# Performance work log

Hardware: AMD Instinct MI355X
Metric: run time of the kernel (lower is better)

The kernel has to match this reference:

```python
import jax, jax.numpy as jnp
import numpy as np

B, C_IN, C_KEY, C_VAL, C_OUT = 1, 64, 32, 64, 64
H = W = D = 64
SCALE = 8


def setup_inputs() -> dict:
    key = jax.random.key(0)
    ks = jax.random.split(key, 4)
    init = lambda k, shape, fan: jax.random.normal(k, shape, jnp.float32) * (fan ** -0.5)
    return {
        "x": jax.random.normal(ks[0], (B, C_IN, H, W, D), jnp.float32),
        "w_key": init(ks[1], (C_KEY, C_IN), C_IN),
        "b_key": jnp.zeros((C_KEY,), jnp.float32),
        "w_value": init(ks[2], (C_VAL, C_IN), C_IN),
        "b_value": jnp.zeros((C_VAL,), jnp.float32),
        "w_out": init(ks[3], (C_OUT, C_VAL), C_VAL),
        "b_out": jnp.zeros((C_OUT,), jnp.float32),
        "scale": SCALE,
    }


def _proj(t, wgt, bias):
    # 1x1x1 Conv3d == pointwise channel matmul
    return jnp.einsum('bchwd,oc->bohwd', t, wgt) + bias[None, :, None, None, None]


def _windows(t, s):
    # [B,C,H,W,D] -> [B, s^3 windows, hb*wb*db tokens, C]
    b, c, h, w, d = t.shape
    hb, wb, db = h // s, w // s, d // s
    t = t.reshape(b, c, s, hb, s, wb, s, db)
    t = t.transpose(0, 2, 4, 6, 3, 5, 7, 1)
    return t.reshape(b, s * s * s, hb * wb * db, c), (hb, wb, db)


def _unwindows(t, s, blk):
    hb, wb, db = blk
    b, c = t.shape[0], t.shape[-1]
    t = t.reshape(b, s, s, s, hb, wb, db, c)
    t = t.transpose(0, 7, 1, 4, 2, 5, 3, 6)
    return t.reshape(b, c, s * hb, s * wb, s * db)


def reference(x, w_key, b_key, w_value, b_value, w_out, b_out, scale):
    # f_query = f_key (shared module in the original)
    k_full = _proj(x, w_key, b_key)
    v_full = _proj(x, w_value, b_value)
    qw, blk = _windows(k_full, scale)
    kw = qw  # shared projection -> query == key
    vw, _ = _windows(v_full, scale)
    sim = jnp.einsum('bnlc,bnmc->bnlm', qw, kw) * (qw.shape[-1] ** -0.5)
    sim = jax.nn.softmax(sim, axis=-1)
    ctx = jnp.einsum('bnlm,bnmc->bnlc', sim, vw)
    ctx = _unwindows(ctx, scale, blk)
    return _proj(ctx, w_out, b_out)
```

## Files before the change

### kernel.cpp

```cpp
#include <hip/hip_runtime.h>

typedef unsigned short u16;
typedef __bf16 bf16x8 __attribute__((ext_vector_type(8)));
typedef float f32x16 __attribute__((ext_vector_type(16)));

union B8 { bf16x8 v; u16 s[8]; unsigned u[4]; uint4 u4; };

__device__ __forceinline__ unsigned cvtpk(float a, float b) {
    unsigned r;
    asm("v_cvt_pk_bf16_f32 %0, %1, %2" : "=v"(r) : "v"(a), "v"(b));
    return r;
}
__device__ __forceinline__ float ex2(float x) { return __builtin_amdgcn_exp2f(x); }
__device__ __forceinline__ void swap32(unsigned &a, unsigned &b) {
    asm("v_permlane32_swap_b32 %0, %1" : "+v"(a), "+v"(b));
}
__device__ __forceinline__ B8 load_w8(const float* __restrict__ p, float s) {
    float4 lo = ((const float4*)p)[0];
    float4 hi = ((const float4*)p)[1];
    B8 r;
    r.u[0] = cvtpk(lo.x * s, lo.y * s);
    r.u[1] = cvtpk(lo.z * s, lo.w * s);
    r.u[2] = cvtpk(hi.x * s, hi.y * s);
    r.u[3] = cvtpk(hi.z * s, hi.w * s);
    return r;
}
__device__ __forceinline__ f32x16 mfma32(const B8 a, const B8 b, f32x16 c) {
    return __builtin_amdgcn_mfma_f32_32x32x16_bf16(a.v, b.v, c, 0, 0, 0);
}
__device__ __forceinline__ int kidx(int row, int sl) {
    return row * 32 + (((sl ^ (row >> 1)) & 3) << 3);
}
__device__ __forceinline__ void build_b(const float* p, B8& b0, B8& b1) {
    unsigned c0 = cvtpk(p[0], p[1]),   c1 = cvtpk(p[2], p[3]);
    unsigned c2 = cvtpk(p[4], p[5]),   c3 = cvtpk(p[6], p[7]);
    unsigned c4 = cvtpk(p[8], p[9]),   c5 = cvtpk(p[10], p[11]);
    unsigned c6 = cvtpk(p[12], p[13]), c7 = cvtpk(p[14], p[15]);
    swap32(c0, c2); swap32(c1, c3); swap32(c4, c6); swap32(c5, c7);
    b0.u[0] = c0; b0.u[1] = c1; b0.u[2] = c2; b0.u[3] = c3;
    b1.u[0] = c4; b1.u[1] = c5; b1.u[2] = c6; b1.u[3] = c7;
}

#define VOFF 16384
#define XOFF 49664
#define NSM  68096

__global__ __launch_bounds__(512, 1)
void psab_fused(const float* __restrict__ x,
                const float* __restrict__ wk, const float* __restrict__ bk,
                const float* __restrict__ wv, const float* __restrict__ bv,
                const float* __restrict__ wo, const float* __restrict__ bo,
                float* __restrict__ out)
{
    __shared__ __align__(16) u16 smem[NSM];
    const int t    = threadIdx.x;
    const int lane = t & 63;
    const int wid  = t >> 6;
    const int cl   = lane & 31;
    const int h5   = lane >> 5;

    const int bid = blockIdx.x;
    const int n   = (bid & 7) * 64 + (bid >> 3);
    const int sh = n >> 6, sw = (n >> 3) & 7, sd = n & 7;
    const size_t base_vox = (size_t)(sh * 8) * 4096 + (size_t)(sw * 8) * 64 + (size_t)(sd * 8);

    const float WSC = 0.50506330f;

    B8 wkB[4], wvB[2][4];
#pragma unroll
    for (int kc = 0; kc < 4; ++kc)
        wkB[kc] = load_w8(wk + cl * 64 + kc * 16 + h5 * 8, WSC);
#pragma unroll
    for (int nb = 0; nb < 2; ++nb)
#pragma unroll
        for (int kc = 0; kc < 4; ++kc)
            wvB[nb][kc] = load_w8(wv + (nb * 32 + cl) * 64 + kc * 16 + h5 * 8, 1.0f);
    const float kbias = bk[cl] * WSC;
    const float vbias[2] = { bv[cl], bv[32 + cl] };

    const f32x16 z16 = {0,0,0,0,0,0,0,0,0,0,0,0,0,0,0,0};

    const int cS = t & 63;
    const int r2 = t >> 6;
    float4 L4[4], H4[4];
#define LDX(cc)                                                                              \
    _Pragma("unroll")                                                                        \
    for (int i = 0; i < 4; ++i) {                                                            \
        const float* gp = x + (size_t)cS * 262144 + base_vox + ((cc) * 4 + i) * 4096 + r2 * 64; \
        L4[i] = ((const float4*)gp)[0];                                                      \
        H4[i] = ((const float4*)gp)[1];                                                      \
    }
#define STX()                                                                                \
    _Pragma("unroll")                                                                        \
    for (int i = 0; i < 4; ++i) {                                                            \
        unsigned a0 = cvtpk(L4[i].x, L4[i].y), a1 = cvtpk(L4[i].z, L4[i].w);                 \
        unsigned a2 = cvtpk(H4[i].x, H4[i].y), a3 = cvtpk(H4[i].z, H4[i].w);                 \
        u16* xp = &smem[XOFF + (i * 64 + r2 * 8) * 72 + cS];                                 \
        xp[0 * 72] = (u16)a0; xp[1 * 72] = (u16)(a0 >> 16);                                  \
        xp[2 * 72] = (u16)a1; xp[3 * 72] = (u16)(a1 >> 16);                                  \
        xp[4 * 72] = (u16)a2; xp[5 * 72] = (u16)(a2 >> 16);                                  \
        xp[6 * 72] = (u16)a3; xp[7 * 72] = (u16)(a3 >> 16);                                  \
    }

    LDX(0)
    STX()
    __syncthreads();
    LDX(1)

#pragma unroll
    for (int cc = 0; cc < 2; ++cc) {
        const int tokb = cc * 256 + wid * 32;
        B8 ax[4];
#pragma unroll
        for (int kc = 0; kc < 4; ++kc)
            ax[kc].u4 = *(const uint4*)&smem[XOFF + (wid * 32 + cl) * 72 + kc * 16 + h5 * 8];
        f32x16 kd = mfma32(ax[0], wkB[0], z16);
        kd = mfma32(ax[1], wkB[1], kd);
        kd = mfma32(ax[2], wkB[2], kd);
        kd = mfma32(ax[3], wkB[3], kd);
#pragma unroll
        for (int r = 0; r < 16; ++r) {
            const int row = tokb + (r & 3) + 8 * (r >> 2) + 4 * h5;
            smem[kidx(row, cl >> 3) + (cl & 7)] = (u16)cvtpk(kd[r] + kbias, kd[r] + kbias);
        }
#pragma unroll
        for (int nb = 0; nb < 2; ++nb) {
            f32x16 vd = mfma32(ax[0], wvB[nb][0], z16);
            vd = mfma32(ax[1], wvB[nb][1], vd);
            vd = mfma32(ax[2], wvB[nb][2], vd);
            vd = mfma32(ax[3], wvB[nb][3], vd);
            const int cv = nb * 32 + cl;
            const float vb = vbias[nb];
#pragma unroll
            for (int rq = 0; rq < 4; ++rq) {
                uint2 pk;
                pk.x = cvtpk(vd[rq * 4 + 0] + vb, vd[rq * 4 + 1] + vb);
                pk.y = cvtpk(vd[rq * 4 + 2] + vb, vd[rq * 4 + 3] + vb);
                *(uint2*)&smem[VOFF + cv * 520 + tokb + rq * 8 + 4 * h5] = pk;
            }
        }
        if (cc == 0) {
            __syncthreads();
            STX()
            __syncthreads();
        }
    }
    __syncthreads();

    B8 qB[2][2];
#pragma unroll
    for (int qb = 0; qb < 2; ++qb)
#pragma unroll
        for (int kc = 0; kc < 2; ++kc)
            qB[qb][kc].u4 = *(const uint4*)&smem[kidx(wid * 64 + qb * 32 + cl, 2 * kc + h5)];

    f32x16 ctx00 = z16, ctx01 = z16, ctx10 = z16, ctx11 = z16;
    float lsum0 = 0.f, lsum1 = 0.f;

#pragma unroll 2
    for (int ci = 0; ci < 16; ++ci) {
        const int m0 = ci * 32;
        B8 kA0, kA1, va00, va01, va10, va11;
        kA0.u4 = *(const uint4*)&smem[kidx(m0 + cl, h5)];
        kA1.u4 = *(const uint4*)&smem[kidx(m0 + cl, 2 + h5)];
        va00.u4 = *(const uint4*)&smem[VOFF + cl * 520 + m0 + h5 * 8];
        va01.u4 = *(const uint4*)&smem[VOFF + cl * 520 + m0 + 16 + h5 * 8];
        va10.u4 = *(const uint4*)&smem[VOFF + (32 + cl) * 520 + m0 + h5 * 8];
        va11.u4 = *(const uint4*)&smem[VOFF + (32 + cl) * 520 + m0 + 16 + h5 * 8];

        f32x16 s0 = mfma32(kA0, qB[0][0], z16);
        s0 = mfma32(kA1, qB[0][1], s0);
        f32x16 s1 = mfma32(kA0, qB[1][0], z16);
        s1 = mfma32(kA1, qB[1][1], s1);

        float p[16];
        B8 pb00, pb01, pb10, pb11;
#pragma unroll
        for (int i = 0; i < 16; ++i) p[i] = ex2(s0[i]);
        lsum0 += (((p[0]+p[1])+(p[2]+p[3]))+((p[4]+p[5])+(p[6]+p[7])))
               + (((p[8]+p[9])+(p[10]+p[11]))+((p[12]+p[13])+(p[14]+p[15])));
        build_b(p, pb00, pb01);
#pragma unroll
        for (int i = 0; i < 16; ++i) p[i] = ex2(s1[i]);
        lsum1 += (((p[0]+p[1])+(p[2]+p[3]))+((p[4]+p[5])+(p[6]+p[7])))
               + (((p[8]+p[9])+(p[10]+p[11]))+((p[12]+p[13])+(p[14]+p[15])));
        build_b(p, pb10, pb11);

        ctx00 = mfma32(va00, pb00, ctx00); ctx00 = mfma32(va01, pb01, ctx00);
        ctx10 = mfma32(va10, pb00, ctx10); ctx10 = mfma32(va11, pb01, ctx10);
        ctx01 = mfma32(va00, pb10, ctx01); ctx01 = mfma32(va01, pb11, ctx01);
        ctx11 = mfma32(va10, pb10, ctx11); ctx11 = mfma32(va11, pb11, ctx11);
    }

    lsum0 += __shfl_xor(lsum0, 32);
    lsum1 += __shfl_xor(lsum1, 32);
    const float inv0 = 1.0f / lsum0;
    const float inv1 = 1.0f / lsum1;

    B8 aw[2][4];
#pragma unroll
    for (int cob = 0; cob < 2; ++cob)
#pragma unroll
        for (int kc = 0; kc < 4; ++kc)
            aw[cob][kc] = load_w8(wo + (cob * 32 + cl) * 64 + kc * 16 + h5 * 8, 1.0f);

    float pn[16];
    B8 cq0[4], cq1[4];
#pragma unroll
    for (int i = 0; i < 16; ++i) pn[i] = ctx00[i] * inv0;
    build_b(pn, cq0[0], cq0[1]);
#pragma unroll
    for (int i = 0; i < 16; ++i) pn[i] = ctx10[i] * inv0;
    build_b(pn, cq0[2], cq0[3]);
#pragma unroll
    for (int i = 0; i < 16; ++i) pn[i] = ctx01[i] * inv1;
    build_b(pn, cq1[0], cq1[1]);
#pragma unroll
    for (int i = 0; i < 16; ++i) pn[i] = ctx11[i] * inv1;
    build_b(pn, cq1[2], cq1[3]);

    __syncthreads();

    float* fout = (float*)((char*)smem + wid * 16384);
#pragma unroll
    for (int cob = 0; cob < 2; ++cob) {
        f32x16 od0 = mfma32(aw[cob][0], cq0[0], z16);
        od0 = mfma32(aw[cob][1], cq0[1], od0);
        od0 = mfma32(aw[cob][2], cq0[2], od0);
        od0 = mfma32(aw[cob][3], cq0[3], od0);
        f32x16 od1 = mfma32(aw[cob][0], cq1[0], z16);
        od1 = mfma32(aw[cob][1], cq1[1], od1);
        od1 = mfma32(aw[cob][2], cq1[2], od1);
        od1 = mfma32(aw[cob][3], cq1[3], od1);
#pragma unroll
        for (int rq = 0; rq < 4; ++rq) {
            const float4 b4 = *(const float4*)(bo + cob * 32 + rq * 8 + h5 * 4);
            const float bb[4] = { b4.x, b4.y, b4.z, b4.w };
#pragma unroll
            for (int i = 0; i < 4; ++i) {
                const int row = cob * 32 + rq * 8 + h5 * 4 + i;
                fout[row * 64 + cl]      = od0[rq * 4 + i] + bb[i];
                fout[row * 64 + 32 + cl] = od1[rq * 4 + i] + bb[i];
            }
        }
    }

    float* outw = out + base_vox + (size_t)wid * 4096;
    const int lq = lane >> 4, lr = lane & 15;
#pragma unroll
    for (int it = 0; it < 16; ++it) {
        const int co = it * 4 + lq;
        const float4 v4 = *(const float4*)&fout[co * 64 + lr * 4];
        const int wb = lr >> 1, db0 = (lr & 1) * 4;
        *(float4*)&outw[(size_t)co * 262144 + wb * 64 + db0] = v4;
    }
}

extern "C" void kernel_launch(void* const* d_in, const int* in_sizes, int n_in,
                              void* d_out, int out_size, void* d_ws, size_t ws_size,
                              hipStream_t stream) {
    const float* x  = (const float*)d_in[0];
    const float* wk = (const float*)d_in[1];
    const float* bk = (const float*)d_in[2];
    const float* wv = (const float*)d_in[3];
    const float* bv = (const float*)d_in[4];
    const float* wo = (const float*)d_in[5];
    const float* bo = (const float*)d_in[6];
    float* o = (float*)d_out;
    psab_fused<<<dim3(512), dim3(512), 0, stream>>>(x, wk, bk, wv, bv, wo, bo, o);
}
```

Before: 72.34 us.

## Double block to 1024 threads, split K/V projection across wave pairs

Launches 1024 threads per block, so each wave handles 32 query rows instead of 64. In the projection phase, wave pairs divide the work: even waves compute K and odd waves compute V. The change also adds s_setprio around the MFMA groups and moves the output bias add into the store loop. It aims to raise wave-level parallelism and latency hiding, at the cost of more barrier participants and duplicated X fragment loads.

```diff
diff --git a/kernel.cpp b/kernel.cpp
--- a/kernel.cpp
+++ b/kernel.cpp
@@ -45,7 +45,7 @@
 #define XOFF 49664
 #define NSM  68096
 
-__global__ __launch_bounds__(512, 1)
+__global__ __launch_bounds__(1024, 4)
 void psab_fused(const float* __restrict__ x,
                 const float* __restrict__ wk, const float* __restrict__ bk,
                 const float* __restrict__ wv, const float* __restrict__ bv,
@@ -66,40 +66,53 @@
 
     const float WSC = 0.50506330f;
 
-    B8 wkB[4], wvB[2][4];
-#pragma unroll
-    for (int kc = 0; kc < 4; ++kc)
-        wkB[kc] = load_w8(wk + cl * 64 + kc * 16 + h5 * 8, WSC);
-#pragma unroll
-    for (int nb = 0; nb < 2; ++nb)
+    const int pair = wid >> 1;
+    const int kv   = wid & 1;
+
+    B8 wB[8];
+    float bkv[16];
+    float vb0 = 0.f, vb1 = 0.f;
+    if (kv == 0) {
 #pragma unroll
         for (int kc = 0; kc < 4; ++kc)
-            wvB[nb][kc] = load_w8(wv + (nb * 32 + cl) * 64 + kc * 16 + h5 * 8, 1.0f);
-    const float kbias = bk[cl] * WSC;
-    const float vbias[2] = { bv[cl], bv[32 + cl] };
+            wB[kc] = load_w8(wk + cl * 64 + kc * 16 + h5 * 8, WSC);
+#pragma unroll
+        for (int r = 0; r < 16; ++r)
+            bkv[r] = bk[(r & 3) + 8 * (r >> 2) + 4 * h5] * WSC;
+    } else {
+#pragma unroll
+        for (int nb = 0; nb < 2; ++nb)
+#pragma unroll
+            for (int kc = 0; kc < 4; ++kc)
+                wB[nb * 4 + kc] = load_w8(wv + (nb * 32 + cl) * 64 + kc * 16 + h5 * 8, 1.0f);
+        vb0 = bv[cl]; vb1 = bv[32 + cl];
+    }
 
     const f32x16 z16 = {0,0,0,0,0,0,0,0,0,0,0,0,0,0,0,0};
 
     const int cS = t & 63;
-    const int r2 = t >> 6;
-    float4 L4[4], H4[4];
-#define LDX(cc)                                                                              \
-    _Pragma("unroll")                                                                        \
-    for (int i = 0; i < 4; ++i) {                                                            \
-        const float* gp = x + (size_t)cS * 262144 + base_vox + ((cc) * 4 + i) * 4096 + r2 * 64; \
-        L4[i] = ((const float4*)gp)[0];                                                      \
-        H4[i] = ((const float4*)gp)[1];                                                      \
-    }
-#define STX()                                                                                \
-    _Pragma("unroll")                                                                        \
-    for (int i = 0; i < 4; ++i) {                                                            \
-        unsigned a0 = cvtpk(L4[i].x, L4[i].y), a1 = cvtpk(L4[i].z, L4[i].w);                 \
-        unsigned a2 = cvtpk(H4[i].x, H4[i].y), a3 = cvtpk(H4[i].z, H4[i].w);                 \
-        u16* xp = &smem[XOFF + (i * 64 + r2 * 8) * 72 + cS];                                 \
-        xp[0 * 72] = (u16)a0; xp[1 * 72] = (u16)(a0 >> 16);                                  \
-        xp[2 * 72] = (u16)a1; xp[3 * 72] = (u16)(a1 >> 16);                                  \
-        xp[4 * 72] = (u16)a2; xp[5 * 72] = (u16)(a2 >> 16);                                  \
-        xp[6 * 72] = (u16)a3; xp[7 * 72] = (u16)(a3 >> 16);                                  \
+    const int r3 = t >> 6;
+    float4 L4[2], H4[2];
+#define LDX(cc)                                                                               \
+    _Pragma("unroll")                                                                         \
+    for (int i = 0; i < 2; ++i) {                                                             \
+        const int rr = r3 + i * 16;                                                           \
+        const float* gp = x + (size_t)cS * 262144 + base_vox                                  \
+                        + ((cc) * 4 + (rr >> 3)) * 4096 + (rr & 7) * 64;                      \
+        L4[i] = ((const float4*)gp)[0];                                                       \
+        H4[i] = ((const float4*)gp)[1];                                                       \
+    }
+#define STX()                                                                                 \
+    _Pragma("unroll")                                                                         \
+    for (int i = 0; i < 2; ++i) {                                                             \
+        const int rr = r3 + i * 16;                                                           \
+        unsigned a0 = cvtpk(L4[i].x, L4[i].y), a1 = cvtpk(L4[i].z, L4[i].w);                  \
+        unsigned a2 = cvtpk(H4[i].x, H4[i].y), a3 = cvtpk(H4[i].z, H4[i].w);                  \
+        u16* xp = &smem[XOFF + (rr * 8) * 72 + cS];                                           \
+        xp[0 * 72] = (u16)a0; xp[1 * 72] = (u16)(a0 >> 16);                                   \
+        xp[2 * 72] = (u16)a1; xp[3 * 72] = (u16)(a1 >> 16);                                   \
+        xp[4 * 72] = (u16)a2; xp[5 * 72] = (u16)(a2 >> 16);                                   \
+        xp[6 * 72] = (u16)a3; xp[7 * 72] = (u16)(a3 >> 16);                                   \
     }
 
     LDX(0)
@@ -109,34 +122,40 @@
 
 #pragma unroll
     for (int cc = 0; cc < 2; ++cc) {
-        const int tokb = cc * 256 + wid * 32;
+        const int tokb = cc * 256 + pair * 32;
         B8 ax[4];
 #pragma unroll
         for (int kc = 0; kc < 4; ++kc)
-            ax[kc].u4 = *(const uint4*)&smem[XOFF + (wid * 32 + cl) * 72 + kc * 16 + h5 * 8];
-        f32x16 kd = mfma32(ax[0], wkB[0], z16);
-        kd = mfma32(ax[1], wkB[1], kd);
-        kd = mfma32(ax[2], wkB[2], kd);
-        kd = mfma32(ax[3], wkB[3], kd);
-#pragma unroll
-        for (int r = 0; r < 16; ++r) {
-            const int row = tokb + (r & 3) + 8 * (r >> 2) + 4 * h5;
-            smem[kidx(row, cl >> 3) + (cl & 7)] = (u16)cvtpk(kd[r] + kbias, kd[r] + kbias);
-        }
-#pragma unroll
-        for (int nb = 0; nb < 2; ++nb) {
-            f32x16 vd = mfma32(ax[0], wvB[nb][0], z16);
-            vd = mfma32(ax[1], wvB[nb][1], vd);
-            vd = mfma32(ax[2], wvB[nb][2], vd);
-            vd = mfma32(ax[3], wvB[nb][3], vd);
-            const int cv = nb * 32 + cl;
-            const float vb = vbias[nb];
-#pragma unroll
-            for (int rq = 0; rq < 4; ++rq) {
+            ax[kc].u4 = *(const uint4*)&smem[XOFF + (pair * 32 + cl) * 72 + kc * 16 + h5 * 8];
+        if (kv == 0) {
+            f32x16 kd = mfma32(wB[0], ax[0], z16);
+            kd = mfma32(wB[1], ax[1], kd);
+            kd = mfma32(wB[2], ax[2], kd);
+            kd = mfma32(wB[3], ax[3], kd);
+            const int trow = tokb + cl;
+#pragma unroll
+            for (int g = 0; g < 4; ++g) {
                 uint2 pk;
-                pk.x = cvtpk(vd[rq * 4 + 0] + vb, vd[rq * 4 + 1] + vb);
-                pk.y = cvtpk(vd[rq * 4 + 2] + vb, vd[rq * 4 + 3] + vb);
-                *(uint2*)&smem[VOFF + cv * 520 + tokb + rq * 8 + 4 * h5] = pk;
+                pk.x = cvtpk(kd[4 * g + 0] + bkv[4 * g + 0], kd[4 * g + 1] + bkv[4 * g + 1]);
+                pk.y = cvtpk(kd[4 * g + 2] + bkv[4 * g + 2], kd[4 * g + 3] + bkv[4 * g + 3]);
+                *(uint2*)&smem[kidx(trow, g) + 4 * h5] = pk;
+            }
+        } else {
+#pragma unroll
+            for (int nb = 0; nb < 2; ++nb) {
+                f32x16 vd = mfma32(ax[0], wB[nb * 4 + 0], z16);
+                vd = mfma32(ax[1], wB[nb * 4 + 1], vd);
+                vd = mfma32(ax[2], wB[nb * 4 + 2], vd);
+                vd = mfma32(ax[3], wB[nb * 4 + 3], vd);
+                const int cv = nb * 32 + cl;
+                const float vb = nb ? vb1 : vb0;
+#pragma unroll
+                for (int rq = 0; rq < 4; ++rq) {
+                    uint2 pk;
+                    pk.x = cvtpk(vd[rq * 4 + 0] + vb, vd[rq * 4 + 1] + vb);
+                    pk.y = cvtpk(vd[rq * 4 + 2] + vb, vd[rq * 4 + 3] + vb);
+                    *(uint2*)&smem[VOFF + cv * 520 + tokb + rq * 8 + 4 * h5] = pk;
+                }
             }
         }
         if (cc == 0) {
@@ -147,55 +166,48 @@
     }
     __syncthreads();
 
-    B8 qB[2][2];
-#pragma unroll
-    for (int qb = 0; qb < 2; ++qb)
-#pragma unroll
-        for (int kc = 0; kc < 2; ++kc)
-            qB[qb][kc].u4 = *(const uint4*)&smem[kidx(wid * 64 + qb * 32 + cl, 2 * kc + h5)];
-
-    f32x16 ctx00 = z16, ctx01 = z16, ctx10 = z16, ctx11 = z16;
-    float lsum0 = 0.f, lsum1 = 0.f;
+    B8 qB[2];
+#pragma unroll
+    for (int kc = 0; kc < 2; ++kc)
+        qB[kc].u4 = *(const uint4*)&smem[kidx(wid * 32 + cl, 2 * kc + h5)];
+
+    f32x16 ctx0 = z16, ctx1 = z16;
+    float lsum = 0.f;
 
 #pragma unroll 2
     for (int ci = 0; ci < 16; ++ci) {
         const int m0 = ci * 32;
         B8 kA0, kA1, va00, va01, va10, va11;
-        kA0.u4 = *(const uint4*)&smem[kidx(m0 + cl, h5)];
-        kA1.u4 = *(const uint4*)&smem[kidx(m0 + cl, 2 + h5)];
+        kA0.u4  = *(const uint4*)&smem[kidx(m0 + cl, h5)];
+        kA1.u4  = *(const uint4*)&smem[kidx(m0 + cl, 2 + h5)];
         va00.u4 = *(const uint4*)&smem[VOFF + cl * 520 + m0 + h5 * 8];
         va01.u4 = *(const uint4*)&smem[VOFF + cl * 520 + m0 + 16 + h5 * 8];
         va10.u4 = *(const uint4*)&smem[VOFF + (32 + cl) * 520 + m0 + h5 * 8];
         va11.u4 = *(const uint4*)&smem[VOFF + (32 + cl) * 520 + m0 + 16 + h5 * 8];
 
-        f32x16 s0 = mfma32(kA0, qB[0][0], z16);
-        s0 = mfma32(kA1, qB[0][1], s0);
-        f32x16 s1 = mfma32(kA0, qB[1][0], z16);
-        s1 = mfma32(kA1, qB[1][1], s1);
+        __builtin_amdgcn_s_setprio(1);
+        f32x16 s = mfma32(kA0, qB[0], z16);
+        s = mfma32(kA1, qB[1], s);
+        __builtin_amdgcn_s_setprio(0);
 
         float p[16];
-        B8 pb00, pb01, pb10, pb11;
-#pragma unroll
-        for (int i = 0; i < 16; ++i) p[i] = ex2(s0[i]);
-        lsum0 += (((p[0]+p[1])+(p[2]+p[3]))+((p[4]+p[5])+(p[6]+p[7])))
-               + (((p[8]+p[9])+(p[10]+p[11]))+((p[12]+p[13])+(p[14]+p[15])));
-        build_b(p, pb00, pb01);
-#pragma unroll
-        for (int i = 0; i < 16; ++i) p[i] = ex2(s1[i]);
-        lsum1 += (((p[0]+p[1])+(p[2]+p[3]))+((p[4]+p[5])+(p[6]+p[7])))
-               + (((p[8]+p[9])+(p[10]+p[11]))+((p[12]+p[13])+(p[14]+p[15])));
-        build_b(p, pb10, pb11);
-
-        ctx00 = mfma32(va00, pb00, ctx00); ctx00 = mfma32(va01, pb01, ctx00);
-        ctx10 = mfma32(va10, pb00, ctx10); ctx10 = mfma32(va11, pb01, ctx10);
-        ctx01 = mfma32(va00, pb10, ctx01); ctx01 = mfma32(va01, pb11, ctx01);
-        ctx11 = mfma32(va10, pb10, ctx11); ctx11 = mfma32(va11, pb11, ctx11);
-    }
-
-    lsum0 += __shfl_xor(lsum0, 32);
-    lsum1 += __shfl_xor(lsum1, 32);
-    const float inv0 = 1.0f / lsum0;
-    const float inv1 = 1.0f / lsum1;
+#pragma unroll
+        for (int i = 0; i < 16; ++i) p[i] = ex2(s[i]);
+        lsum += (((p[0]+p[1])+(p[2]+p[3]))+((p[4]+p[5])+(p[6]+p[7])))
+              + (((p[8]+p[9])+(p[10]+p[11]))+((p[12]+p[13])+(p[14]+p[15])));
+        B8 pb0, pb1;
+        build_b(p, pb0, pb1);
+
+        __builtin_amdgcn_s_setprio(1);
+        ctx0 = mfma32(va00, pb0, ctx0);
+        ctx0 = mfma32(va01, pb1, ctx0);
+        ctx1 = mfma32(va10, pb0, ctx1);
+        ctx1 = mfma32(va11, pb1, ctx1);
+        __builtin_amdgcn_s_setprio(0);
+    }
+
+    lsum += __shfl_xor(lsum, 32);
+    const float inv = 1.0f / lsum;
 
     B8 aw[2][4];
 #pragma unroll
@@ -205,53 +217,39 @@
             aw[cob][kc] = load_w8(wo + (cob * 32 + cl) * 64 + kc * 16 + h5 * 8, 1.0f);
 
     float pn[16];
-    B8 cq0[4], cq1[4];
-#pragma unroll
-    for (int i = 0; i < 16; ++i) pn[i] = ctx00[i] * inv0;
-    build_b(pn, cq0[0], cq0[1]);
-#pragma unroll
-    for (int i = 0; i < 16; ++i) pn[i] = ctx10[i] * inv0;
-    build_b(pn, cq0[2], cq0[3]);
-#pragma unroll
-    for (int i = 0; i < 16; ++i) pn[i] = ctx01[i] * inv1;
-    build_b(pn, cq1[0], cq1[1]);
-#pragma unroll
-    for (int i = 0; i < 16; ++i) pn[i] = ctx11[i] * inv1;
-    build_b(pn, cq1[2], cq1[3]);
+    B8 cq[4];
+#pragma unroll
+    for (int i = 0; i < 16; ++i) pn[i] = ctx0[i] * inv;
+    build_b(pn, cq[0], cq[1]);
+#pragma unroll
+    for (int i = 0; i < 16; ++i) pn[i] = ctx1[i] * inv;
+    build_b(pn, cq[2], cq[3]);
 
     __syncthreads();
 
-    float* fout = (float*)((char*)smem + wid * 16384);
+    float* fout = (float*)((char*)smem + wid * 8192);
 #pragma unroll
     for (int cob = 0; cob < 2; ++cob) {
-        f32x16 od0 = mfma32(aw[cob][0], cq0[0], z16);
-        od0 = mfma32(aw[cob][1], cq0[1], od0);
-        od0 = mfma32(aw[cob][2], cq0[2], od0);
-        od0 = mfma32(aw[cob][3], cq0[3], od0);
-        f32x16 od1 = mfma32(aw[cob][0], cq1[0], z16);
-        od1 = mfma32(aw[cob][1], cq1[1], od1);
-        od1 = mfma32(aw[cob][2], cq1[2], od1);
-        od1 = mfma32(aw[cob][3], cq1[3], od1);
-#pragma unroll
-        for (int rq = 0; rq < 4; ++rq) {
-            const float4 b4 = *(const float4*)(bo + cob * 32 + rq * 8 + h5 * 4);
-            const float bb[4] = { b4.x, b4.y, b4.z, b4.w };
-#pragma unroll
-            for (int i = 0; i < 4; ++i) {
-                const int row = cob * 32 + rq * 8 + h5 * 4 + i;
-                fout[row * 64 + cl]      = od0[rq * 4 + i] + bb[i];
-                fout[row * 64 + 32 + cl] = od1[rq * 4 + i] + bb[i];
-            }
+        f32x16 od = mfma32(aw[cob][0], cq[0], z16);
+        od = mfma32(aw[cob][1], cq[1], od);
+        od = mfma32(aw[cob][2], cq[2], od);
+        od = mfma32(aw[cob][3], cq[3], od);
+#pragma unroll
+        for (int r = 0; r < 16; ++r) {
+            const int row = cob * 32 + (r & 3) + 8 * (r >> 2) + 4 * h5;
+            fout[row * 32 + cl] = od[r];
         }
     }
 
-    float* outw = out + base_vox + (size_t)wid * 4096;
-    const int lq = lane >> 4, lr = lane & 15;
-#pragma unroll
-    for (int it = 0; it < 16; ++it) {
-        const int co = it * 4 + lq;
-        const float4 v4 = *(const float4*)&fout[co * 64 + lr * 4];
-        const int wb = lr >> 1, db0 = (lr & 1) * 4;
+    float* outw = out + base_vox + (size_t)(wid >> 1) * 4096 + (wid & 1) * 256;
+#pragma unroll
+    for (int it = 0; it < 8; ++it) {
+        const int co = it * 8 + (lane >> 3);
+        const int q4 = (lane & 7) * 4;
+        float4 v4 = *(const float4*)&fout[co * 32 + q4];
+        const float bco = bo[co];
+        v4.x += bco; v4.y += bco; v4.z += bco; v4.w += bco;
+        const int wb = (lane & 7) >> 1, db0 = (lane & 1) * 4;
         *(float4*)&outw[(size_t)co * 262144 + wb * 64 + db0] = v4;
     }
 }
@@ -267,5 +265,5 @@
     const float* wo = (const float*)d_in[5];
     const float* bo = (const float*)d_in[6];
     float* o = (float*)d_out;
-    psab_fused<<<dim3(512), dim3(512), 0, stream>>>(x, wk, bk, wv, bv, wo, bo, o);
-}
+    psab_fused<<<dim3(512), dim3(1024), 0, stream>>>(x, wk, bk, wv, bv, wo, bo, o);
+}
```

Result: slower. 74.32 us (+2.7%).

## Offload softmax row sums to MFMA and emulate part of exp2 on VALU

Applied to the files above, without the earlier changes.

Row sums of the softmax are now computed with an MFMA against a ones matrix rather than VALU adds plus a cross-half shuffle. Three of every sixteen exponentials use a polynomial exp2 on the ALU to take load off the transcendental unit. The key projection is transposed so K is written to shared memory as packed 64-bit stores instead of scalar 16-bit stores. The change also adds s_setprio around MFMA groups, stops unrolling the main loop, and moves the output bias add to the store phase. The polynomial exp2 is less accurate, and the extra MFMAs add work on the matrix pipe.

```diff
diff --git a/kernel.cpp b/kernel.cpp
--- a/kernel.cpp
+++ b/kernel.cpp
@@ -12,6 +12,15 @@
     return r;
 }
 __device__ __forceinline__ float ex2(float x) { return __builtin_amdgcn_exp2f(x); }
+__device__ __forceinline__ float ex2p(float x) {
+    float n = floorf(x);
+    float f = x - n;
+    float p = fmaf(f, 0.0802449f, 0.224368f);
+    p = fmaf(f, p, 0.695348f);
+    p = fmaf(f, p, 1.0f);
+    int e = ((int)n + 127) << 23;
+    return __int_as_float(e) * p;
+}
 __device__ __forceinline__ void swap32(unsigned &a, unsigned &b) {
     asm("v_permlane32_swap_b32 %0, %1" : "+v"(a), "+v"(b));
 }
@@ -66,16 +75,19 @@
 
     const float WSC = 0.50506330f;
 
-    B8 wkB[4], wvB[2][4];
+    B8 wkA[4], wvB[2][4];
 #pragma unroll
     for (int kc = 0; kc < 4; ++kc)
-        wkB[kc] = load_w8(wk + cl * 64 + kc * 16 + h5 * 8, WSC);
+        wkA[kc] = load_w8(wk + cl * 64 + kc * 16 + h5 * 8, WSC);
 #pragma unroll
     for (int nb = 0; nb < 2; ++nb)
 #pragma unroll
         for (int kc = 0; kc < 4; ++kc)
             wvB[nb][kc] = load_w8(wv + (nb * 32 + cl) * 64 + kc * 16 + h5 * 8, 1.0f);
-    const float kbias = bk[cl] * WSC;
+    float bkv[16];
+#pragma unroll
+    for (int r = 0; r < 16; ++r)
+        bkv[r] = bk[(r & 3) + 8 * (r >> 2) + 4 * h5] * WSC;
     const float vbias[2] = { bv[cl], bv[32 + cl] };
 
     const f32x16 z16 = {0,0,0,0,0,0,0,0,0,0,0,0,0,0,0,0};
@@ -114,14 +126,17 @@
 #pragma unroll
         for (int kc = 0; kc < 4; ++kc)
             ax[kc].u4 = *(const uint4*)&smem[XOFF + (wid * 32 + cl) * 72 + kc * 16 + h5 * 8];
-        f32x16 kd = mfma32(ax[0], wkB[0], z16);
-        kd = mfma32(ax[1], wkB[1], kd);
-        kd = mfma32(ax[2], wkB[2], kd);
-        kd = mfma32(ax[3], wkB[3], kd);
-#pragma unroll
-        for (int r = 0; r < 16; ++r) {
-            const int row = tokb + (r & 3) + 8 * (r >> 2) + 4 * h5;
-            smem[kidx(row, cl >> 3) + (cl & 7)] = (u16)cvtpk(kd[r] + kbias, kd[r] + kbias);
+        f32x16 kd = mfma32(wkA[0], ax[0], z16);
+        kd = mfma32(wkA[1], ax[1], kd);
+        kd = mfma32(wkA[2], ax[2], kd);
+        kd = mfma32(wkA[3], ax[3], kd);
+        const int trow = tokb + cl;
+#pragma unroll
+        for (int g = 0; g < 4; ++g) {
+            uint2 pk;
+            pk.x = cvtpk(kd[4 * g + 0] + bkv[4 * g + 0], kd[4 * g + 1] + bkv[4 * g + 1]);
+            pk.y = cvtpk(kd[4 * g + 2] + bkv[4 * g + 2], kd[4 * g + 3] + bkv[4 * g + 3]);
+            *(uint2*)&smem[kidx(trow, g) + 4 * h5] = pk;
         }
 #pragma unroll
         for (int nb = 0; nb < 2; ++nb) {
@@ -154,48 +169,53 @@
         for (int kc = 0; kc < 2; ++kc)
             qB[qb][kc].u4 = *(const uint4*)&smem[kidx(wid * 64 + qb * 32 + cl, 2 * kc + h5)];
 
+    B8 ones;
+    ones.u[0] = 0x3f803f80u; ones.u[1] = 0x3f803f80u;
+    ones.u[2] = 0x3f803f80u; ones.u[3] = 0x3f803f80u;
+
     f32x16 ctx00 = z16, ctx01 = z16, ctx10 = z16, ctx11 = z16;
-    float lsum0 = 0.f, lsum1 = 0.f;
-
-#pragma unroll 2
+    f32x16 lacc0 = z16, lacc1 = z16;
+
+#define SM(sv, lac, c0, c1)                                                                   \
+    {                                                                                         \
+        float p[16];                                                                          \
+        _Pragma("unroll")                                                                     \
+        for (int i2 = 0; i2 < 13; ++i2) p[i2] = ex2(sv[i2]);                                  \
+        p[13] = ex2p(sv[13]); p[14] = ex2p(sv[14]); p[15] = ex2p(sv[15]);                     \
+        B8 pb0, pb1;                                                                          \
+        build_b(p, pb0, pb1);                                                                 \
+        __builtin_amdgcn_s_setprio(1);                                                        \
+        lac = mfma32(ones, pb0, lac);                                                         \
+        lac = mfma32(ones, pb1, lac);                                                         \
+        c0 = mfma32(va00, pb0, c0);                                                           \
+        c0 = mfma32(va01, pb1, c0);                                                           \
+        c1 = mfma32(va10, pb0, c1);                                                           \
+        c1 = mfma32(va11, pb1, c1);                                                           \
+        __builtin_amdgcn_s_setprio(0);                                                        \
+    }
+
+#pragma unroll 1
     for (int ci = 0; ci < 16; ++ci) {
         const int m0 = ci * 32;
         B8 kA0, kA1, va00, va01, va10, va11;
-        kA0.u4 = *(const uint4*)&smem[kidx(m0 + cl, h5)];
-        kA1.u4 = *(const uint4*)&smem[kidx(m0 + cl, 2 + h5)];
+        kA0.u4  = *(const uint4*)&smem[kidx(m0 + cl, h5)];
+        kA1.u4  = *(const uint4*)&smem[kidx(m0 + cl, 2 + h5)];
         va00.u4 = *(const uint4*)&smem[VOFF + cl * 520 + m0 + h5 * 8];
         va01.u4 = *(const uint4*)&smem[VOFF + cl * 520 + m0 + 16 + h5 * 8];
         va10.u4 = *(const uint4*)&smem[VOFF + (32 + cl) * 520 + m0 + h5 * 8];
         va11.u4 = *(const uint4*)&smem[VOFF + (32 + cl) * 520 + m0 + 16 + h5 * 8];
 
-        f32x16 s0 = mfma32(kA0, qB[0][0], z16);
-        s0 = mfma32(kA1, qB[0][1], s0);
-        f32x16 s1 = mfma32(kA0, qB[1][0], z16);
-        s1 = mfma32(kA1, qB[1][1], s1);
-
-        float p[16];
-        B8 pb00, pb01, pb10, pb11;
-#pragma unroll
-        for (int i = 0; i < 16; ++i) p[i] = ex2(s0[i]);
-        lsum0 += (((p[0]+p[1])+(p[2]+p[3]))+((p[4]+p[5])+(p[6]+p[7])))
-               + (((p[8]+p[9])+(p[10]+p[11]))+((p[12]+p[13])+(p[14]+p[15])));
-        build_b(p, pb00, pb01);
-#pragma unroll
-        for (int i = 0; i < 16; ++i) p[i] = ex2(s1[i]);
-        lsum1 += (((p[0]+p[1])+(p[2]+p[3]))+((p[4]+p[5])+(p[6]+p[7])))
-               + (((p[8]+p[9])+(p[10]+p[11]))+((p[12]+p[13])+(p[14]+p[15])));
-        build_b(p, pb10, pb11);
-
-        ctx00 = mfma32(va00, pb00, ctx00); ctx00 = mfma32(va01, pb01, ctx00);
-        ctx10 = mfma32(va10, pb00, ctx10); ctx10 = mfma32(va11, pb01, ctx10);
-        ctx01 = mfma32(va00, pb10, ctx01); ctx01 = mfma32(va01, pb11, ctx01);
-        ctx11 = mfma32(va10, pb10, ctx11); ctx11 = mfma32(va11, pb11, ctx11);
-    }
-
-    lsum0 += __shfl_xor(lsum0, 32);
-    lsum1 += __shfl_xor(lsum1, 32);
-    const float inv0 = 1.0f / lsum0;
-    const float inv1 = 1.0f / lsum1;
+        __builtin_amdgcn_s_setprio(1);
+        f32x16 s0 = mfma32(kA0, qB[0][0], z16); s0 = mfma32(kA1, qB[0][1], s0);
+        f32x16 s1 = mfma32(kA0, qB[1][0], z16); s1 = mfma32(kA1, qB[1][1], s1);
+        __builtin_amdgcn_s_setprio(0);
+
+        SM(s0, lacc0, ctx00, ctx01)
+        SM(s1, lacc1, ctx10, ctx11)
+    }
+
+    const float inv0 = 1.0f / lacc0[0];
+    const float inv1 = 1.0f / lacc1[0];
 
     B8 aw[2][4];
 #pragma unroll
@@ -210,10 +230,10 @@
     for (int i = 0; i < 16; ++i) pn[i] = ctx00[i] * inv0;
     build_b(pn, cq0[0], cq0[1]);
 #pragma unroll
-    for (int i = 0; i < 16; ++i) pn[i] = ctx10[i] * inv0;
+    for (int i = 0; i < 16; ++i) pn[i] = ctx01[i] * inv0;
     build_b(pn, cq0[2], cq0[3]);
 #pragma unroll
-    for (int i = 0; i < 16; ++i) pn[i] = ctx01[i] * inv1;
+    for (int i = 0; i < 16; ++i) pn[i] = ctx10[i] * inv1;
     build_b(pn, cq1[0], cq1[1]);
 #pragma unroll
     for (int i = 0; i < 16; ++i) pn[i] = ctx11[i] * inv1;
@@ -233,15 +253,10 @@
         od1 = mfma32(aw[cob][2], cq1[2], od1);
         od1 = mfma32(aw[cob][3], cq1[3], od1);
 #pragma unroll
-        for (int rq = 0; rq < 4; ++rq) {
-            const float4 b4 = *(const float4*)(bo + cob * 32 + rq * 8 + h5 * 4);
-            const float bb[4] = { b4.x, b4.y, b4.z, b4.w };
-#pragma unroll
-            for (int i = 0; i < 4; ++i) {
-                const int row = cob * 32 + rq * 8 + h5 * 4 + i;
-                fout[row * 64 + cl]      = od0[rq * 4 + i] + bb[i];
-                fout[row * 64 + 32 + cl] = od1[rq * 4 + i] + bb[i];
-            }
+        for (int r = 0; r < 16; ++r) {
+            const int row = cob * 32 + (r & 3) + 8 * (r >> 2) + 4 * h5;
+            fout[row * 64 + cl]      = od0[r];
+            fout[row * 64 + 32 + cl] = od1[r];
         }
     }
 
@@ -250,7 +265,9 @@
 #pragma unroll
     for (int it = 0; it < 16; ++it) {
         const int co = it * 4 + lq;
-        const float4 v4 = *(const float4*)&fout[co * 64 + lr * 4];
+        float4 v4 = *(const float4*)&fout[co * 64 + lr * 4];
+        const float bco = bo[co];
+        v4.x += bco; v4.y += bco; v4.z += bco; v4.w += bco;
         const int wb = lr >> 1, db0 = (lr & 1) * 4;
         *(float4*)&outw[(size_t)co * 262144 + wb * 64 + db0] = v4;
     }
```

After: 76.05 us. 1.05x slower.
